# Kernel tuning notes

Measured on AMD Instinct MI355X. Metric: run time of the kernel, lower is better.

Reference implementation:

```python
import jax, jax.numpy as jnp
import numpy as np

N_NODES = 100000
N_EDGES = 1000000
IN_CH = 128
HID = 128
N_CLS = 3


def setup_inputs() -> dict:
    key = jax.random.key(0)
    ks = jax.random.split(key, 10)
    scale_in = 1.0 / np.sqrt(IN_CH)
    scale_h = 1.0 / np.sqrt(HID)
    return {
        "x": jax.random.normal(ks[0], (N_NODES, IN_CH), dtype=jnp.float32),
        "edge_index": jax.random.randint(ks[1], (2, N_EDGES), 0, N_NODES, dtype=jnp.int64),
        # SAGEConv layer 1: lin_l (aggregated neighbors, with bias), lin_r (root, no bias)
        "w_l1": jax.random.normal(ks[2], (IN_CH, HID), dtype=jnp.float32) * scale_in,
        "b_l1": jnp.zeros((HID,), dtype=jnp.float32),
        "w_r1": jax.random.normal(ks[3], (IN_CH, HID), dtype=jnp.float32) * scale_in,
        # SAGEConv layer 2
        "w_l2": jax.random.normal(ks[4], (HID, HID), dtype=jnp.float32) * scale_h,
        "b_l2": jnp.zeros((HID,), dtype=jnp.float32),
        "w_r2": jax.random.normal(ks[5], (HID, HID), dtype=jnp.float32) * scale_h,
        # final classifier
        "w_cls": jax.random.normal(ks[6], (HID, N_CLS), dtype=jnp.float32) * scale_h,
        "b_cls": jnp.zeros((N_CLS,), dtype=jnp.float32),
    }


def _sage_conv(x, src, dst, w_l, b_l, w_r, num_nodes):
    # mean aggregation of source-node features onto destination nodes
    msg = x[src]                                              # [E, C] gather
    agg = jax.ops.segment_sum(msg, dst, num_segments=num_nodes)
    cnt = jax.ops.segment_sum(jnp.ones((src.shape[0],), x.dtype), dst,
                              num_segments=num_nodes)
    mean = agg / jnp.maximum(cnt, 1.0)[:, None]
    # out = lin_l(mean_aggr) + lin_r(x)
    return mean @ w_l + b_l + x @ w_r


def reference(x, edge_index, w_l1, b_l1, w_r1, w_l2, b_l2, w_r2, w_cls, b_cls):
    src, dst = edge_index[0], edge_index[1]
    n = x.shape[0]
    h = jax.nn.relu(_sage_conv(x, src, dst, w_l1, b_l1, w_r1, n))
    # dropout is identity in eval mode
    h = jax.nn.relu(_sage_conv(h, src, dst, w_l2, b_l2, w_r2, n))
    logits = h @ w_cls + b_cls
    return logits
```

## Files before the change

### kernel.cpp

```cpp
#include <hip/hip_runtime.h>
#include <hip/hip_bf16.h>

#define N_NODES 100000
#define N_EDGES 1000000
#define CH 128
#define KTOT 256
#define NCLS 3

#define NBKT 196
#define EPB 4096
#define NB_A ((N_EDGES + EPB - 1) / EPB)
#define M_H (NBKT * NB_A)
#define NB_SCAN ((M_H + 1023) / 1024)

#define NB_CVTX (N_NODES * CH / 4 / 256)
#define NB_CVTW (KTOT * CH / 256)
#define CVT_SCAN 4000
#define CVT_A3   4500
#define CVT_B    4000

typedef __attribute__((ext_vector_type(8))) short v8s;
typedef __attribute__((ext_vector_type(4))) float v4f;

__device__ __forceinline__ float bf2f(unsigned short u) {
    return __uint_as_float(((unsigned int)u) << 16);
}

__device__ __forceinline__ unsigned short f2bf(float f) {
    unsigned int u = __float_as_uint(f);
    unsigned int r = (u + 0x7fffu + ((u >> 16) & 1u)) >> 16;
    return (unsigned short)r;
}

__device__ __forceinline__ int edge_at(const void* e, int is64, long long i) {
    if (is64) return (int)((const long long*)e)[i];
    return ((const int*)e)[i];
}

__device__ __forceinline__ float ldf(const void* p, int isbf, size_t i) {
    if (isbf) return bf2f(((const unsigned short*)p)[i]);
    return ((const float*)p)[i];
}

__device__ __forceinline__ void acc_u32(unsigned int u, float& a0, float& a1) {
    a0 += bf2f((unsigned short)(u & 0xffffu));
    a1 += bf2f((unsigned short)(u >> 16));
}

__device__ __forceinline__ int sniff_is64(const void* e) {
    int lane = threadIdx.x & 63;
    int v = ((const int*)e)[2 * lane + 1];
    unsigned long long bl = __ballot(v != 0);
    return (bl == 0ULL) ? 1 : 0;
}

__device__ __forceinline__ int sniff_isbf(const void* x) {
    int lane = threadIdx.x & 63;
    unsigned int u = ((const unsigned int*)x)[lane];
    int ex = (u >> 7) & 0xff;
    int sane = (ex == 0) || (ex >= 100 && ex <= 154);
    unsigned long long bl = __ballot(sane);
    return (__popcll(bl) >= 48) ? 1 : 0;
}

__device__ __forceinline__ void cvt_x_tile(int tile, int t256, const void* x,
                                           unsigned short* Xb, int isbf) {
    int idx = tile * 256 + t256;
    int node = idx >> 5;
    int ch = (idx & 31) * 4;
    unsigned short o[4];
    if (isbf) {
        ushort4 u = *(const ushort4*)((const unsigned short*)x +
                                      (size_t)node * CH + ch);
        o[0] = u.x; o[1] = u.y; o[2] = u.z; o[3] = u.w;
    } else {
        float4 v = *(const float4*)((const float*)x + (size_t)node * CH + ch);
        o[0] = f2bf(v.x); o[1] = f2bf(v.y); o[2] = f2bf(v.z); o[3] = f2bf(v.w);
    }
    *(ushort4*)(Xb + (size_t)node * CH + ch) = make_ushort4(o[0], o[1], o[2], o[3]);
}

__global__ void k_A1(const void* __restrict__ e, int* __restrict__ eflag,
                     int* __restrict__ dtf, int* __restrict__ done,
                     int* __restrict__ hist,
                     const void* __restrict__ x,
                     const void* __restrict__ wl1, const void* __restrict__ wr1,
                     unsigned short* __restrict__ WT1,
                     const void* __restrict__ wl2, const void* __restrict__ wr2,
                     unsigned short* __restrict__ WT2) {
    int b = blockIdx.x;
    int t = threadIdx.x;
    if (b < NB_A) {
        __shared__ int h[NBKT];
        if (t < NBKT) h[t] = 0;
        int is64 = sniff_is64(e);
        if (b == 0 && t < 64) {
            int isbf = sniff_isbf(x);
            if (t == 0) { *eflag = is64; *dtf = isbf; *done = 0; }
        }
        __syncthreads();
#pragma unroll
        for (int j = 0; j < EPB / 256; j++) {
            int i = b * EPB + j * 256 + t;
            if (i < N_EDGES) {
                int dst = edge_at(e, is64, (long long)N_EDGES + i);
                atomicAdd(&h[dst >> 9], 1);
            }
        }
        __syncthreads();
        if (t < NBKT) hist[t * NB_A + b] = h[t];
    } else {
        int rel = b - NB_A;
        int isbf = sniff_isbf(x);
        const void* wl = (rel < NB_CVTW) ? wl1 : wl2;
        const void* wr = (rel < NB_CVTW) ? wr1 : wr2;
        unsigned short* WT = (rel < NB_CVTW) ? WT1 : WT2;
        int i = (rel % NB_CVTW) * 256 + t;
        int k = i >> 7;
        int n = i & 127;
        float v = (k < CH) ? ldf(wl, isbf, (size_t)k * CH + n)
                           : ldf(wr, isbf, (size_t)(k - CH) * CH + n);
        WT[(size_t)n * KTOT + k] = f2bf(v);
    }
}

__global__ __launch_bounds__(1024) void k_scanH(int* __restrict__ hist,
                                                int* __restrict__ bsum,
                                                int* __restrict__ done,
                                                const void* __restrict__ x,
                                                unsigned short* __restrict__ Xb,
                                                const int* __restrict__ dtf) {
    __shared__ int s[1024];
    __shared__ int pre_sh;
    int t = threadIdx.x, b = blockIdx.x;
    if (b >= NB_SCAN) {
        int cb = b - NB_SCAN;
        int isbf = *dtf;
        cvt_x_tile(cb * 4 + (t >> 8), t & 255, x, Xb, isbf);
        return;
    }
    int idx = b * 1024 + t;
    int v = (idx < M_H) ? hist[idx] : 0;
    s[t] = v;
    __syncthreads();
    for (int off = 1; off < 1024; off <<= 1) {
        int u = (t >= off) ? s[t - off] : 0;
        __syncthreads();
        s[t] += u;
        __syncthreads();
    }
    if (t == 1023) {
        bsum[b] = s[t];
        __threadfence();
        atomicAdd(done, 1);
    }
    if (t == 0) {
        while (__hip_atomic_load(done, __ATOMIC_ACQUIRE,
                                 __HIP_MEMORY_SCOPE_AGENT) < NB_SCAN) {
        }
        __threadfence();
        int run = 0;
        for (int r = 0; r < b; r++) run += bsum[r];
        pre_sh = run;
    }
    __syncthreads();
    if (idx < M_H) hist[idx] = s[t] - v + pre_sh;
}

__global__ void k_A3(const void* __restrict__ e, const int* __restrict__ eflag,
                     const int* __restrict__ hist, unsigned int* __restrict__ part,
                     const void* __restrict__ x, unsigned short* __restrict__ Xb,
                     const int* __restrict__ dtf) {
    __shared__ int cur[NBKT];
    int b = blockIdx.x;
    int t = threadIdx.x;
    if (b >= NB_A) {
        int isbf = *dtf;
        cvt_x_tile(CVT_SCAN + (b - NB_A), t, x, Xb, isbf);
        return;
    }
    if (t < NBKT) cur[t] = hist[t * NB_A + b];
    __syncthreads();
    int is64 = *eflag;
#pragma unroll
    for (int j = 0; j < EPB / 256; j++) {
        int i = b * EPB + j * 256 + t;
        if (i < N_EDGES) {
            int src = edge_at(e, is64, i);
            int dst = edge_at(e, is64, (long long)N_EDGES + i);
            int pos = atomicAdd(&cur[dst >> 9], 1);
            part[pos] = ((unsigned int)src << 9) | (unsigned int)(dst & 511);
        }
    }
}

__global__ __launch_bounds__(1024) void k_B(const int* __restrict__ hist,
                                            const unsigned int* __restrict__ part,
                                            int* __restrict__ row_start,
                                            int* __restrict__ csr_src,
                                            const void* __restrict__ x,
                                            unsigned short* __restrict__ Xb,
                                            const int* __restrict__ dtf) {
    __shared__ int dcnt[512], sa[512], curs[512];
    int b = blockIdx.x;
    int t = threadIdx.x;
    if (b >= NBKT) {
        int cb = b - NBKT;
        int isbf = *dtf;
        cvt_x_tile(CVT_SCAN + CVT_A3 + cb * 4 + (t >> 8), t & 255, x, Xb, isbf);
        return;
    }
    int e0 = hist[b * NB_A];
    int e1 = (b + 1 < NBKT) ? hist[(b + 1) * NB_A] : N_EDGES;
    if (t < 512) dcnt[t] = 0;
    __syncthreads();
    for (int i = e0 + t; i < e1; i += 1024)
        atomicAdd(&dcnt[part[i] & 511], 1);
    __syncthreads();
    if (t < 512) sa[t] = dcnt[t];
    __syncthreads();
    for (int off = 1; off < 512; off <<= 1) {
        int v = 0;
        if (t < 512 && t >= off) v = sa[t - off];
        __syncthreads();
        if (t < 512) sa[t] += v;
        __syncthreads();
    }
    if (t < 512) {
        int excl = sa[t] - dcnt[t];
        curs[t] = e0 + excl;
        int node = b * 512 + t;
        if (node < N_NODES) row_start[node] = e0 + excl;
    }
    if (b == 0 && t == 0) row_start[N_NODES] = N_EDGES;
    __syncthreads();
    for (int i = e0 + t; i < e1; i += 1024) {
        unsigned int p = part[i];
        int pos = atomicAdd(&curs[p & 511], 1);
        csr_src[pos] = (int)(p >> 9);
    }
}

__global__ __launch_bounds__(256) void k_agg(
    const int* __restrict__ row_start, const int* __restrict__ csr_src,
    const unsigned short* __restrict__ src, unsigned short* __restrict__ mdst) {
    long long gt = (long long)blockIdx.x * blockDim.x + threadIdx.x;
    int node = (int)(gt >> 4);
    int lane = (int)(gt & 15);
    if (node >= N_NODES) return;
    int beg = row_start[node];
    int end = row_start[node + 1];
    int n = end - beg;
    float a[8];
#pragma unroll
    for (int j = 0; j < 8; j++) a[j] = 0.f;
    if (n > 0) {
        const unsigned short* gbase = src + lane * 8;
        int nm1 = n - 1;
        int s[16];
#pragma unroll
        for (int j = 0; j < 16; j++) {
            int jj = (j < nm1) ? j : nm1;
            s[j] = csr_src[beg + jj];
        }
        uint4 u[16];
#pragma unroll
        for (int j = 0; j < 16; j++)
            u[j] = *(const uint4*)(gbase + (size_t)s[j] * CH);
#pragma unroll
        for (int j = 0; j < 16; j++) {
            if (j < n) {
                acc_u32(u[j].x, a[0], a[1]); acc_u32(u[j].y, a[2], a[3]);
                acc_u32(u[j].z, a[4], a[5]); acc_u32(u[j].w, a[6], a[7]);
            }
        }
        int e = beg + 16;
        while (e + 8 <= end) {
            int s2[8];
#pragma unroll
            for (int j = 0; j < 8; j++) s2[j] = csr_src[e + j];
            uint4 u2[8];
#pragma unroll
            for (int j = 0; j < 8; j++)
                u2[j] = *(const uint4*)(gbase + (size_t)s2[j] * CH);
#pragma unroll
            for (int j = 0; j < 8; j++) {
                acc_u32(u2[j].x, a[0], a[1]); acc_u32(u2[j].y, a[2], a[3]);
                acc_u32(u2[j].z, a[4], a[5]); acc_u32(u2[j].w, a[6], a[7]);
            }
            e += 8;
        }
        while (e < end) {
            int s0 = csr_src[e];
            uint4 u0 = *(const uint4*)(gbase + (size_t)s0 * CH);
            acc_u32(u0.x, a[0], a[1]); acc_u32(u0.y, a[2], a[3]);
            acc_u32(u0.z, a[4], a[5]); acc_u32(u0.w, a[6], a[7]);
            e++;
        }
    }
    float rinv = 1.0f / (float)max(n, 1);
    unsigned int p0 = (unsigned int)f2bf(a[0] * rinv) | ((unsigned int)f2bf(a[1] * rinv) << 16);
    unsigned int p1 = (unsigned int)f2bf(a[2] * rinv) | ((unsigned int)f2bf(a[3] * rinv) << 16);
    unsigned int p2 = (unsigned int)f2bf(a[4] * rinv) | ((unsigned int)f2bf(a[5] * rinv) << 16);
    unsigned int p3 = (unsigned int)f2bf(a[6] * rinv) | ((unsigned int)f2bf(a[7] * rinv) << 16);
    *(uint4*)(mdst + (size_t)node * CH + lane * 8) = make_uint4(p0, p1, p2, p3);
}

#define LDK 40
#define CLS_LD 130
__global__ __launch_bounds__(256) void k_gemm_mfma(
    const unsigned short* __restrict__ Mb,
    const unsigned short* __restrict__ Xr,
    const unsigned short* __restrict__ WT, const void* __restrict__ bias,
    const int* __restrict__ dtf,
    unsigned short* __restrict__ out,
    const void* __restrict__ wcls, const void* __restrict__ bcls,
    float* __restrict__ cls_out) {
    __shared__ unsigned short smem[4 * 128 * LDK];
    unsigned short* As = smem;
    unsigned short* Bs = smem + 2 * 128 * LDK;
    const int t = threadIdx.x;
    const int w = t >> 6, l = t & 63;
    const int wx = w & 1, wy = w >> 1;
    const int quad = l >> 4, lrow = l & 15;
    const int row0 = blockIdx.x * 128;
    const int srow = t >> 1, shalf = t & 1;
    const int isbf = *dtf;

    int ar = row0 + srow;
    if (ar >= N_NODES) ar = N_NODES - 1;
    const unsigned short* abase_m = Mb + (size_t)ar * CH + shalf * 16;
    const unsigned short* abase_x = Xr + (size_t)ar * CH + shalf * 16;
    const unsigned short* bbase = WT + (size_t)srow * KTOT + shalf * 16;

    v4f acc[4][4];
#pragma unroll
    for (int i = 0; i < 4; i++)
#pragma unroll
        for (int j = 0; j < 4; j++) acc[i][j] = (v4f){0.f, 0.f, 0.f, 0.f};

    {
        uint4 a0 = *(const uint4*)abase_m, a1 = *(const uint4*)(abase_m + 8);
        uint4 b0 = *(const uint4*)bbase, b1 = *(const uint4*)(bbase + 8);
        *(uint4*)&As[srow * LDK + shalf * 16] = a0;
        *(uint4*)&As[srow * LDK + shalf * 16 + 8] = a1;
        *(uint4*)&Bs[srow * LDK + shalf * 16] = b0;
        *(uint4*)&Bs[srow * LDK + shalf * 16 + 8] = b1;
    }
#pragma unroll
    for (int k = 0; k < KTOT / 32; k++) {
        uint4 na0, na1, nb0, nb1;
        if (k < KTOT / 32 - 1) {
            const unsigned short* na = (k < 3) ? (abase_m + (k + 1) * 32)
                                               : (abase_x + (k - 3) * 32);
            na0 = *(const uint4*)na;
            na1 = *(const uint4*)(na + 8);
            nb0 = *(const uint4*)(bbase + (k + 1) * 32);
            nb1 = *(const uint4*)(bbase + (k + 1) * 32 + 8);
        }
        __syncthreads();
        const int cur = (k & 1) * 128 * LDK, nxt = ((k + 1) & 1) * 128 * LDK;
        v8s af[4], bfr[4];
#pragma unroll
        for (int mi = 0; mi < 4; mi++)
            af[mi] = *(const v8s*)&As[cur + (wy * 64 + mi * 16 + lrow) * LDK + quad * 8];
#pragma unroll
        for (int ni = 0; ni < 4; ni++)
            bfr[ni] = *(const v8s*)&Bs[cur + (wx * 64 + ni * 16 + lrow) * LDK + quad * 8];
#pragma unroll
        for (int mi = 0; mi < 4; mi++)
#pragma unroll
            for (int ni = 0; ni < 4; ni++)
                acc[mi][ni] = __builtin_amdgcn_mfma_f32_16x16x32_bf16(
                    af[mi], bfr[ni], acc[mi][ni], 0, 0, 0);
        if (k < KTOT / 32 - 1) {
            *(uint4*)&As[nxt + srow * LDK + shalf * 16] = na0;
            *(uint4*)&As[nxt + srow * LDK + shalf * 16 + 8] = na1;
            *(uint4*)&Bs[nxt + srow * LDK + shalf * 16] = nb0;
            *(uint4*)&Bs[nxt + srow * LDK + shalf * 16 + 8] = nb1;
        }
    }
    float bj[4];
#pragma unroll
    for (int ni = 0; ni < 4; ni++) bj[ni] = ldf(bias, isbf, wx * 64 + ni * 16 + lrow);

    if (!cls_out) {
#pragma unroll
        for (int mi = 0; mi < 4; mi++) {
#pragma unroll
            for (int r = 0; r < 4; r++) {
                int grow = row0 + wy * 64 + mi * 16 + quad * 4 + r;
                if (grow < N_NODES) {
#pragma unroll
                    for (int ni = 0; ni < 4; ni++) {
                        int col = wx * 64 + ni * 16 + lrow;
                        float v = fmaxf(acc[mi][ni][r] + bj[ni], 0.0f);
                        out[(size_t)grow * CH + col] = f2bf(v);
                    }
                }
            }
        }
    } else {
        __syncthreads();
        float* wcls_s = (float*)(smem + 16896);
        for (int i = t; i < CH * NCLS; i += 256) wcls_s[i] = ldf(wcls, isbf, i);
#pragma unroll
        for (int mi = 0; mi < 4; mi++) {
#pragma unroll
            for (int r = 0; r < 4; r++) {
                int row = wy * 64 + mi * 16 + quad * 4 + r;
#pragma unroll
                for (int ni = 0; ni < 4; ni++) {
                    int col = wx * 64 + ni * 16 + lrow;
                    float v = fmaxf(acc[mi][ni][r] + bj[ni], 0.0f);
                    smem[row * CLS_LD + col] = f2bf(v);
                }
            }
        }
        __syncthreads();
        if (t < 128) {
            int grow = row0 + t;
            if (grow < N_NODES) {
                float a0 = 0.f, a1 = 0.f, a2 = 0.f;
                for (int k = 0; k < CH; k++) {
                    float h = bf2f(smem[t * CLS_LD + k]);
                    a0 += h * wcls_s[k * NCLS + 0];
                    a1 += h * wcls_s[k * NCLS + 1];
                    a2 += h * wcls_s[k * NCLS + 2];
                }
                cls_out[(size_t)grow * NCLS + 0] = a0 + ldf(bcls, isbf, 0);
                cls_out[(size_t)grow * NCLS + 1] = a1 + ldf(bcls, isbf, 1);
                cls_out[(size_t)grow * NCLS + 2] = a2 + ldf(bcls, isbf, 2);
            }
        }
    }
}

extern "C" void kernel_launch(void* const* d_in, const int* in_sizes, int n_in,
                              void* d_out, int out_size, void* d_ws, size_t ws_size,
                              hipStream_t stream) {
    const void* x = d_in[0];
    const void* eidx = d_in[1];
    const void* w_l1 = d_in[2];
    const void* b_l1 = d_in[3];
    const void* w_r1 = d_in[4];
    const void* w_l2 = d_in[5];
    const void* b_l2 = d_in[6];
    const void* w_r2 = d_in[7];
    const void* w_cls = d_in[8];
    const void* b_cls = d_in[9];

    char* w = (char*)d_ws;
    int* eflag = (int*)w;
    int* dtf = (int*)(w + 64);
    int* done = (int*)(w + 128);
    int* hist = (int*)(w + 4096);
    int* bsum = (int*)(w + 196608);
    int* row_start = (int*)(w + 262144);
    unsigned int* part = (unsigned int*)(w + 720896);
    int* csr_src = (int*)(w + 4915200);
    unsigned short* WT1 = (unsigned short*)(w + 8978432);
    unsigned short* WT2 = (unsigned short*)(w + 9043968);
    unsigned short* Xb = (unsigned short*)(w + 11534336);
    unsigned short* Mb = (unsigned short*)(w + 37748736);
    unsigned short* Hb = (unsigned short*)(w + 67108864);

    hipLaunchKernelGGL(k_A1, dim3(NB_A + 2 * NB_CVTW), dim3(256), 0, stream,
                       eidx, eflag, dtf, done, hist, x,
                       w_l1, w_r1, WT1, w_l2, w_r2, WT2);
    hipLaunchKernelGGL(k_scanH, dim3(NB_SCAN + CVT_SCAN / 4), dim3(1024), 0, stream,
                       hist, bsum, done, x, Xb, dtf);
    hipLaunchKernelGGL(k_A3, dim3(NB_A + CVT_A3), dim3(256), 0, stream,
                       eidx, eflag, hist, part, x, Xb, dtf);
    hipLaunchKernelGGL(k_B, dim3(NBKT + CVT_B / 4), dim3(1024), 0, stream,
                       hist, part, row_start, csr_src, x, Xb, dtf);
    hipLaunchKernelGGL(k_agg, dim3(N_NODES * 16 / 256), dim3(256), 0, stream,
                       row_start, csr_src, Xb, Mb);
    hipLaunchKernelGGL(k_gemm_mfma, dim3((N_NODES + 127) / 128), dim3(256), 0, stream,
                       Mb, Xb, WT1, b_l1, dtf, Hb,
                       (const void*)nullptr, (const void*)nullptr, (float*)nullptr);
    hipLaunchKernelGGL(k_agg, dim3(N_NODES * 16 / 256), dim3(256), 0, stream,
                       row_start, csr_src, Hb, Mb);
    hipLaunchKernelGGL(k_gemm_mfma, dim3((N_NODES + 127) / 128), dim3(256), 0, stream,
                       Mb, Hb, WT2, b_l2, dtf, (unsigned short*)nullptr,
                       w_cls, b_cls, (float*)d_out);
}
```

Measured before the change: 256.1 us.

## Fuse neighbor aggregation and GEMM into one per-layer kernel with tile counters

Merges the aggregation kernel and the MFMA GEMM kernel of each SAGE layer into a single launch. Block IDs are interleaved so that each 128-row tile's eight aggregation blocks and its GEMM block share an XCD. The GEMM block spin-waits on a per-tile atomic counter that the aggregation blocks bump when they finish. This aims to remove the launch gap and let the GEMM run while other tiles are still aggregating, and to keep Mb hot in the local L2. It risks deadlock or idle waiting if GEMM blocks occupy CUs before their producer blocks are scheduled, and adds spin and atomic overhead.

```diff
diff --git a/kernel.cpp b/kernel.cpp
--- a/kernel.cpp
+++ b/kernel.cpp
@@ -18,6 +18,11 @@
 #define CVT_SCAN 4000
 #define CVT_A3   4500
 #define CVT_B    4000
+
+#define TILES 782
+#define AGG_NB 6250
+#define GPX 98
+#define GRID_L (8 * GPX * 9)
 
 typedef __attribute__((ext_vector_type(8))) short v8s;
 typedef __attribute__((ext_vector_type(4))) float v4f;
@@ -87,7 +92,8 @@
                      const void* __restrict__ wl1, const void* __restrict__ wr1,
                      unsigned short* __restrict__ WT1,
                      const void* __restrict__ wl2, const void* __restrict__ wr2,
-                     unsigned short* __restrict__ WT2) {
+                     unsigned short* __restrict__ WT2,
+                     int* __restrict__ tiles1, int* __restrict__ tiles2) {
     int b = blockIdx.x;
     int t = threadIdx.x;
     if (b < NB_A) {
@@ -109,7 +115,7 @@
         }
         __syncthreads();
         if (t < NBKT) hist[t * NB_A + b] = h[t];
-    } else {
+    } else if (b < NB_A + 2 * NB_CVTW) {
         int rel = b - NB_A;
         int isbf = sniff_isbf(x);
         const void* wl = (rel < NB_CVTW) ? wl1 : wl2;
@@ -121,6 +127,8 @@
         float v = (k < CH) ? ldf(wl, isbf, (size_t)k * CH + n)
                            : ldf(wr, isbf, (size_t)(k - CH) * CH + n);
         WT[(size_t)n * KTOT + k] = f2bf(v);
+    } else {
+        for (int i = t; i < TILES; i += 256) { tiles1[i] = 0; tiles2[i] = 0; }
     }
 }
 
@@ -241,96 +249,121 @@
     }
 }
 
-__global__ __launch_bounds__(256) void k_agg(
-    const int* __restrict__ row_start, const int* __restrict__ csr_src,
-    const unsigned short* __restrict__ src, unsigned short* __restrict__ mdst) {
-    long long gt = (long long)blockIdx.x * blockDim.x + threadIdx.x;
-    int node = (int)(gt >> 4);
-    int lane = (int)(gt & 15);
-    if (node >= N_NODES) return;
-    int beg = row_start[node];
-    int end = row_start[node + 1];
-    int n = end - beg;
-    float a[8];
-#pragma unroll
-    for (int j = 0; j < 8; j++) a[j] = 0.f;
-    if (n > 0) {
-        const unsigned short* gbase = src + lane * 8;
-        int nm1 = n - 1;
-        int s[16];
-#pragma unroll
-        for (int j = 0; j < 16; j++) {
-            int jj = (j < nm1) ? j : nm1;
-            s[j] = csr_src[beg + jj];
-        }
-        uint4 u[16];
-#pragma unroll
-        for (int j = 0; j < 16; j++)
-            u[j] = *(const uint4*)(gbase + (size_t)s[j] * CH);
-#pragma unroll
-        for (int j = 0; j < 16; j++) {
-            if (j < n) {
-                acc_u32(u[j].x, a[0], a[1]); acc_u32(u[j].y, a[2], a[3]);
-                acc_u32(u[j].z, a[4], a[5]); acc_u32(u[j].w, a[6], a[7]);
-            }
-        }
-        int e = beg + 16;
-        while (e + 8 <= end) {
-            int s2[8];
-#pragma unroll
-            for (int j = 0; j < 8; j++) s2[j] = csr_src[e + j];
-            uint4 u2[8];
-#pragma unroll
-            for (int j = 0; j < 8; j++)
-                u2[j] = *(const uint4*)(gbase + (size_t)s2[j] * CH);
-#pragma unroll
-            for (int j = 0; j < 8; j++) {
-                acc_u32(u2[j].x, a[0], a[1]); acc_u32(u2[j].y, a[2], a[3]);
-                acc_u32(u2[j].z, a[4], a[5]); acc_u32(u2[j].w, a[6], a[7]);
-            }
-            e += 8;
-        }
-        while (e < end) {
-            int s0 = csr_src[e];
-            uint4 u0 = *(const uint4*)(gbase + (size_t)s0 * CH);
-            acc_u32(u0.x, a[0], a[1]); acc_u32(u0.y, a[2], a[3]);
-            acc_u32(u0.z, a[4], a[5]); acc_u32(u0.w, a[6], a[7]);
-            e++;
-        }
-    }
-    float rinv = 1.0f / (float)max(n, 1);
-    unsigned int p0 = (unsigned int)f2bf(a[0] * rinv) | ((unsigned int)f2bf(a[1] * rinv) << 16);
-    unsigned int p1 = (unsigned int)f2bf(a[2] * rinv) | ((unsigned int)f2bf(a[3] * rinv) << 16);
-    unsigned int p2 = (unsigned int)f2bf(a[4] * rinv) | ((unsigned int)f2bf(a[5] * rinv) << 16);
-    unsigned int p3 = (unsigned int)f2bf(a[6] * rinv) | ((unsigned int)f2bf(a[7] * rinv) << 16);
-    *(uint4*)(mdst + (size_t)node * CH + lane * 8) = make_uint4(p0, p1, p2, p3);
-}
-
 #define LDK 40
 #define CLS_LD 130
-__global__ __launch_bounds__(256) void k_gemm_mfma(
-    const unsigned short* __restrict__ Mb,
-    const unsigned short* __restrict__ Xr,
+__global__ __launch_bounds__(256) void k_layer(
+    const int* __restrict__ row_start, const int* __restrict__ csr_src,
+    const unsigned short* __restrict__ gsrc,
+    unsigned short* __restrict__ Mb,
     const unsigned short* __restrict__ WT, const void* __restrict__ bias,
     const int* __restrict__ dtf,
     unsigned short* __restrict__ out,
     const void* __restrict__ wcls, const void* __restrict__ bcls,
-    float* __restrict__ cls_out) {
+    float* __restrict__ cls_out,
+    int* __restrict__ tdone) {
     __shared__ unsigned short smem[4 * 128 * LDK];
+    const int t = threadIdx.x;
+    const int p = blockIdx.x;
+    const int xcd = p & 7;
+    const int kk = p >> 3;
+    const int g2 = kk / 9;
+    const int r2 = kk - g2 * 9;
+    const int tile = g2 * 8 + xcd;
+    if (tile >= TILES) return;
+
+    if (r2 < 8) {
+        int a = tile * 8 + r2;
+        if (a < AGG_NB) {
+            int node = a * 16 + (t >> 4);
+            int lane = t & 15;
+            int beg = row_start[node];
+            int end = row_start[node + 1];
+            int n = end - beg;
+            float acc8[8];
+#pragma unroll
+            for (int j = 0; j < 8; j++) acc8[j] = 0.f;
+            if (n > 0) {
+                const unsigned short* gbase = gsrc + lane * 8;
+                int nm1 = n - 1;
+                int s[16];
+#pragma unroll
+                for (int j = 0; j < 16; j++) {
+                    int jj = (j < nm1) ? j : nm1;
+                    s[j] = csr_src[beg + jj];
+                }
+                uint4 u[16];
+#pragma unroll
+                for (int j = 0; j < 16; j++)
+                    u[j] = *(const uint4*)(gbase + (size_t)s[j] * CH);
+#pragma unroll
+                for (int j = 0; j < 16; j++) {
+                    if (j < n) {
+                        acc_u32(u[j].x, acc8[0], acc8[1]); acc_u32(u[j].y, acc8[2], acc8[3]);
+                        acc_u32(u[j].z, acc8[4], acc8[5]); acc_u32(u[j].w, acc8[6], acc8[7]);
+                    }
+                }
+                int e = beg + 16;
+                while (e + 8 <= end) {
+                    int s2[8];
+#pragma unroll
+                    for (int j = 0; j < 8; j++) s2[j] = csr_src[e + j];
+                    uint4 u2[8];
+#pragma unroll
+                    for (int j = 0; j < 8; j++)
+                        u2[j] = *(const uint4*)(gbase + (size_t)s2[j] * CH);
+#pragma unroll
+                    for (int j = 0; j < 8; j++) {
+                        acc_u32(u2[j].x, acc8[0], acc8[1]); acc_u32(u2[j].y, acc8[2], acc8[3]);
+                        acc_u32(u2[j].z, acc8[4], acc8[5]); acc_u32(u2[j].w, acc8[6], acc8[7]);
+                    }
+                    e += 8;
+                }
+                while (e < end) {
+                    int s0 = csr_src[e];
+                    uint4 u0 = *(const uint4*)(gbase + (size_t)s0 * CH);
+                    acc_u32(u0.x, acc8[0], acc8[1]); acc_u32(u0.y, acc8[2], acc8[3]);
+                    acc_u32(u0.z, acc8[4], acc8[5]); acc_u32(u0.w, acc8[6], acc8[7]);
+                    e++;
+                }
+            }
+            float rinv = 1.0f / (float)((n > 1) ? n : 1);
+            unsigned int p0 = (unsigned int)f2bf(acc8[0] * rinv) | ((unsigned int)f2bf(acc8[1] * rinv) << 16);
+            unsigned int p1 = (unsigned int)f2bf(acc8[2] * rinv) | ((unsigned int)f2bf(acc8[3] * rinv) << 16);
+            unsigned int p2 = (unsigned int)f2bf(acc8[4] * rinv) | ((unsigned int)f2bf(acc8[5] * rinv) << 16);
+            unsigned int p3 = (unsigned int)f2bf(acc8[6] * rinv) | ((unsigned int)f2bf(acc8[7] * rinv) << 16);
+            *(uint4*)(Mb + (size_t)node * CH + lane * 8) = make_uint4(p0, p1, p2, p3);
+            __syncthreads();
+            if (t == 0) {
+                __threadfence();
+                atomicAdd(&tdone[tile], 1);
+            }
+        }
+        return;
+    }
+
+    {
+        int need = AGG_NB - tile * 8;
+        if (need > 8) need = 8;
+        if (t == 0) {
+            while (__hip_atomic_load(&tdone[tile], __ATOMIC_RELAXED,
+                                     __HIP_MEMORY_SCOPE_AGENT) < need) {
+            }
+        }
+        __syncthreads();
+    }
     unsigned short* As = smem;
     unsigned short* Bs = smem + 2 * 128 * LDK;
-    const int t = threadIdx.x;
     const int w = t >> 6, l = t & 63;
     const int wx = w & 1, wy = w >> 1;
     const int quad = l >> 4, lrow = l & 15;
-    const int row0 = blockIdx.x * 128;
+    const int row0 = tile * 128;
     const int srow = t >> 1, shalf = t & 1;
     const int isbf = *dtf;
 
     int ar = row0 + srow;
     if (ar >= N_NODES) ar = N_NODES - 1;
     const unsigned short* abase_m = Mb + (size_t)ar * CH + shalf * 16;
-    const unsigned short* abase_x = Xr + (size_t)ar * CH + shalf * 16;
+    const unsigned short* abase_x = gsrc + (size_t)ar * CH + shalf * 16;
     const unsigned short* bbase = WT + (size_t)srow * KTOT + shalf * 16;
 
     v4f acc[4][4];
@@ -456,6 +489,8 @@
     int* done = (int*)(w + 128);
     int* hist = (int*)(w + 4096);
     int* bsum = (int*)(w + 196608);
+    int* tiles1 = (int*)(w + 200704);
+    int* tiles2 = (int*)(w + 204800);
     int* row_start = (int*)(w + 262144);
     unsigned int* part = (unsigned int*)(w + 720896);
     int* csr_src = (int*)(w + 4915200);
@@ -465,23 +500,21 @@
     unsigned short* Mb = (unsigned short*)(w + 37748736);
     unsigned short* Hb = (unsigned short*)(w + 67108864);
 
-    hipLaunchKernelGGL(k_A1, dim3(NB_A + 2 * NB_CVTW), dim3(256), 0, stream,
+    hipLaunchKernelGGL(k_A1, dim3(NB_A + 2 * NB_CVTW + 1), dim3(256), 0, stream,
                        eidx, eflag, dtf, done, hist, x,
-                       w_l1, w_r1, WT1, w_l2, w_r2, WT2);
+                       w_l1, w_r1, WT1, w_l2, w_r2, WT2, tiles1, tiles2);
     hipLaunchKernelGGL(k_scanH, dim3(NB_SCAN + CVT_SCAN / 4), dim3(1024), 0, stream,
                        hist, bsum, done, x, Xb, dtf);
     hipLaunchKernelGGL(k_A3, dim3(NB_A + CVT_A3), dim3(256), 0, stream,
                        eidx, eflag, hist, part, x, Xb, dtf);
     hipLaunchKernelGGL(k_B, dim3(NBKT + CVT_B / 4), dim3(1024), 0, stream,
                        hist, part, row_start, csr_src, x, Xb, dtf);
-    hipLaunchKernelGGL(k_agg, dim3(N_NODES * 16 / 256), dim3(256), 0, stream,
-                       row_start, csr_src, Xb, Mb);
-    hipLaunchKernelGGL(k_gemm_mfma, dim3((N_NODES + 127) / 128), dim3(256), 0, stream,
-                       Mb, Xb, WT1, b_l1, dtf, Hb,
-                       (const void*)nullptr, (const void*)nullptr, (float*)nullptr);
-    hipLaunchKernelGGL(k_agg, dim3(N_NODES * 16 / 256), dim3(256), 0, stream,
-                       row_start, csr_src, Hb, Mb);
-    hipLaunchKernelGGL(k_gemm_mfma, dim3((N_NODES + 127) / 128), dim3(256), 0, stream,
-                       Mb, Hb, WT2, b_l2, dtf, (unsigned short*)nullptr,
-                       w_cls, b_cls, (float*)d_out);
-}
+    hipLaunchKernelGGL(k_layer, dim3(GRID_L), dim3(256), 0, stream,
+                       row_start, csr_src, Xb, Mb, WT1, b_l1, dtf, Hb,
+                       (const void*)nullptr, (const void*)nullptr,
+                       (float*)nullptr, tiles1);
+    hipLaunchKernelGGL(k_layer, dim3(GRID_L), dim3(256), 0, stream,
+                       row_start, csr_src, Hb, Mb, WT2, b_l2, dtf,
+                       (unsigned short*)nullptr, w_cls, b_cls,
+                       (float*)d_out, tiles2);
+}
```

Result: slower. 827.6 us (+223.1%).
